# Optimization experiments

Measured on AMD Instinct MI355X. Metric: run time of the kernel, lower is better.

The kernel has to match this reference:

```python
import jax, jax.numpy as jnp
import numpy as np

B, S, D, K = 8, 2048, 1024, 204  # K = int(0.1 * seq_len)
LN_EPS = 1e-12


def setup_inputs() -> dict:
    key = jax.random.key(0)
    ks = jax.random.split(key, 8)
    scale = 0.02
    return {
        "input_tensor": jax.random.normal(ks[0], (B, S, D), jnp.float32),
        "attention_mask": jnp.zeros((B, 1, 1, S), jnp.float32),  # unused by module
        "Wq": jax.random.normal(ks[1], (D, K), jnp.float32) * scale,
        "bq": jnp.zeros((K,), jnp.float32),
        "Wk": jax.random.normal(ks[2], (D, K), jnp.float32) * scale,
        "bk": jnp.zeros((K,), jnp.float32),
        "Wv": jax.random.normal(ks[3], (D, D), jnp.float32) * scale,
        "bv": jnp.zeros((D,), jnp.float32),
        "Wd": jax.random.normal(ks[4], (D, D), jnp.float32) * scale,
        "bd": jnp.zeros((D,), jnp.float32),
        "gamma": jnp.ones((D,), jnp.float32),
        "beta": jnp.zeros((D,), jnp.float32),
    }


def reference(input_tensor, attention_mask, Wq, bq, Wk, bk, Wv, bv, Wd, bd, gamma, beta):
    # factorized synthesizer: low-rank (k=204) Q/K projections
    q = input_tensor @ Wq + bq          # [B,S,K]
    k = input_tensor @ Wk + bk          # [B,S,K]
    v = input_tensor @ Wv + bv          # [B,S,D]
    scores = jnp.einsum('bsk,btk->bst', q, k)          # [B,S,S]
    probs = jax.nn.softmax(scores, axis=-1)
    # per-head matmul with broadcast probs == direct matmul on merged heads
    ctx = jnp.einsum('bst,btd->bsd', probs, v)          # [B,S,D]
    h = ctx @ Wd + bd
    y = h + input_tensor                                 # residual
    mean = jnp.mean(y, axis=-1, keepdims=True)
    var = jnp.mean(jnp.square(y - mean), axis=-1, keepdims=True)
    return gamma * (y - mean) / jnp.sqrt(var + LN_EPS) + beta
```

## Files before the change

### kernel.cpp

```cpp
#include <hip/hip_runtime.h>
#include <stdint.h>

#define BB 8
#define SS 2048
#define DD 1024
#define KREAL 204

typedef __attribute__((ext_vector_type(8))) short short8;
typedef __attribute__((ext_vector_type(4))) float floatx4;
typedef uint16_t u16;
typedef uint32_t u32;

__device__ __forceinline__ float bf2f(u16 u) {
    union { float f; u32 i; } c; c.i = ((u32)u) << 16; return c.f;
}
__device__ __forceinline__ u16 f2bf(float f) {
    union { float f; u32 i; } c; c.f = f;
    u32 i = c.i;
    u32 r = (i + 0x7FFFu + ((i >> 16) & 1u)) >> 16;
    return (u16)r;
}

#if defined(__has_builtin)
#if __has_builtin(__builtin_amdgcn_global_load_lds)
#define HAVE_GLL 1
#endif
#endif

__device__ __forceinline__ void gload16(const u16* g, u16* l) {
#ifdef HAVE_GLL
    __builtin_amdgcn_global_load_lds(
        (const __attribute__((address_space(1))) void*)(uintptr_t)g,
        (__attribute__((address_space(3))) void*)(u32)(uintptr_t)(void*)l,
        16, 0, 0);
#else
    *(uint4*)l = *(const uint4*)g;
#endif
}

#define VM_WAIT(N) asm volatile("s_waitcnt vmcnt(" #N ")" ::: "memory")
#define S_BAR()    asm volatile("s_barrier" ::: "memory")

__device__ __forceinline__ void stage64(const u16* __restrict__ src, size_t ld,
                                        u16* lds, int tid) {
#pragma unroll
    for (int j = 0; j < 2; j++) {
        int flat = j * 256 + tid;
        int row = flat >> 3, slot = flat & 7;
        int kg = slot ^ (row & 7);
        gload16(src + (size_t)row * ld + kg * 8, lds + flat * 8);
    }
}
__device__ __forceinline__ short8 frag(const u16* lds, int row, int kslot) {
    return *(const short8*)&lds[(row << 6) + (((kslot ^ (row & 7)) & 7) << 3)];
}

__device__ __forceinline__ short8 frag32(const u16* plane, int row, int ks) {
    return *(const short8*)&plane[(row << 5) + (((ks ^ ((row >> 1) & 3)) & 3) << 3)];
}

__device__ __forceinline__ void stage_half(const u16* s0, const u16* s1,
                                           u16* dp, int tid) {
    gload16(s0, dp + tid * 8);
    gload16(s1, dp + 4096 + tid * 8);
}

template <int MT, bool LOADB>
__device__ __forceinline__ void phase16(const u16* Apl, const u16* Bpl,
                                        int arow, int brow, int ln, int quad,
                                        short8 (&bv)[4], floatx4 (&acc)[8][4]) {
    short8 af[4];
#pragma unroll
    for (int i = 0; i < 4; i++) af[i] = frag32(Apl, arow + (MT + i) * 16 + ln, quad);
    if (LOADB) {
#pragma unroll
        for (int nt = 0; nt < 4; nt++) bv[nt] = frag32(Bpl, brow + nt * 16 + ln, quad);
    }
    __builtin_amdgcn_s_setprio(1);
#pragma unroll
    for (int i = 0; i < 4; i++)
#pragma unroll
        for (int nt = 0; nt < 4; nt++)
            acc[MT + i][nt] = __builtin_amdgcn_mfma_f32_16x16x32_bf16(
                af[i], bv[nt], acc[MT + i][nt], 0, 0, 0);
    __builtin_amdgcn_s_setprio(0);
}

template <int NT>
__device__ __forceinline__ void gemm_core256(
    const u16* __restrict__ Ag, size_t lda,
    const u16* __restrict__ Bg, size_t ldb,
    u16* lds, int tid, floatx4 (&acc)[8][4]) {
    const int lane = tid & 63, w = tid >> 6;
    const int arow = (w >> 2) * 128, brow = (w & 3) * 64;
    const int ln = lane & 15, quad = lane >> 4;
    const int srow = tid >> 2;
    const int kgp = (tid & 3) ^ ((srow >> 1) & 3);
    const u16* A0 = Ag + (size_t)srow * lda + kgp * 8;
    const u16* A1 = Ag + (size_t)(srow + 128) * lda + kgp * 8;
    const u16* B0 = Bg + (size_t)srow * ldb + kgp * 8;
    const u16* B1 = Bg + (size_t)(srow + 128) * ldb + kgp * 8;
    u16* Al = lds;
    u16* Bl = lds + 32768;

    stage_half(A0,      A1,      Al,         tid);
    stage_half(B0,      B1,      Bl,         tid);
    stage_half(A0 + 32, A1 + 32, Al + 8192,  tid);
    stage_half(B0 + 32, B1 + 32, Bl + 8192,  tid);
    stage_half(A0 + 64, A1 + 64, Al + 16384, tid);
    stage_half(B0 + 64, B1 + 64, Bl + 16384, tid);

    short8 bv[4];
#pragma unroll 2
    for (int t = 0; t < NT - 1; ++t) {
        const int p  = (t & 1) * 2;
        const int pn = 2 - p;
        const u16* Ap0 = Al + p * 8192;
        const u16* Ap1 = Al + p * 8192 + 8192;
        const u16* Bp0 = Bl + p * 8192;
        const u16* Bp1 = Bl + p * 8192 + 8192;
        const size_t o1 = (size_t)(t + 1) * 64;
        const size_t o2 = (size_t)(t + 2) * 64;
        VM_WAIT(8); S_BAR();
        stage_half(A0 + o1 + 32, A1 + o1 + 32, Al + (pn + 1) * 8192, tid);
        phase16<0, true >(Ap0, Bp0, arow, brow, ln, quad, bv, acc);
        stage_half(B0 + o1 + 32, B1 + o1 + 32, Bl + (pn + 1) * 8192, tid);
        phase16<4, false>(Ap0, Bp0, arow, brow, ln, quad, bv, acc);
        VM_WAIT(8); S_BAR();
        if (t + 2 < NT) stage_half(A0 + o2, A1 + o2, Al + p * 8192, tid);
        phase16<0, true >(Ap1, Bp1, arow, brow, ln, quad, bv, acc);
        if (t + 2 < NT) stage_half(B0 + o2, B1 + o2, Bl + p * 8192, tid);
        phase16<4, false>(Ap1, Bp1, arow, brow, ln, quad, bv, acc);
    }
    {
        const int p = ((NT - 1) & 1) * 2;
        const u16* Ap0 = Al + p * 8192;
        const u16* Ap1 = Al + p * 8192 + 8192;
        const u16* Bp0 = Bl + p * 8192;
        const u16* Bp1 = Bl + p * 8192 + 8192;
        VM_WAIT(4); S_BAR();
        phase16<0, true >(Ap0, Bp0, arow, brow, ln, quad, bv, acc);
        phase16<4, false>(Ap0, Bp0, arow, brow, ln, quad, bv, acc);
        VM_WAIT(0); S_BAR();
        phase16<0, true >(Ap1, Bp1, arow, brow, ln, quad, bv, acc);
        phase16<4, false>(Ap1, Bp1, arow, brow, ln, quad, bv, acc);
    }
}

template <typename F>
__device__ __forceinline__ void store_rm256(u16* smem, u16* gbase, size_t ldc,
                                            int wm, int wn, int ln, int quad,
                                            int tid, F val) {
    for (int half = 0; half < 2; half++) {
        __syncthreads();
        if (wm == half) {
#pragma unroll
            for (int mt = 0; mt < 8; mt++)
#pragma unroll
                for (int nt = 0; nt < 4; nt++)
#pragma unroll
                    for (int r = 0; r < 4; r++)
                        smem[(mt * 16 + quad * 4 + r) * 264 + wn * 64 + nt * 16 + ln] =
                            val(mt, nt, r);
        }
        __syncthreads();
#pragma unroll
        for (int j = 0; j < 8; j++) {
            int flat = j * 512 + tid;
            int row = flat >> 5, c = flat & 31;
            *(uint4*)&gbase[(size_t)(half * 128 + row) * ldc + c * 8] =
                *(const uint4*)&smem[row * 264 + c * 8];
        }
    }
}

template <typename F4>
__device__ __forceinline__ void store_tr256(u16* smem, u16* gbase, size_t ldg,
                                            int wm, int wn, int ln, int quad,
                                            int tid, F4 val4) {
    for (int qr = 0; qr < 4; qr++) {
        __syncthreads();
        if (wn == qr) {
#pragma unroll
            for (int mt = 0; mt < 8; mt++)
#pragma unroll
                for (int nt = 0; nt < 4; nt++) {
                    ushort4 v = val4(mt, nt);
                    *(ushort4*)&smem[(nt * 16 + ln) * 264 + wm * 128 + mt * 16 + quad * 4] = v;
                }
        }
        __syncthreads();
#pragma unroll
        for (int j = 0; j < 4; j++) {
            int flat = j * 512 + tid;
            int c = flat >> 5, r8 = flat & 31;
            *(uint4*)&gbase[(size_t)(qr * 64 + c) * ldg + r8 * 8] =
                *(const uint4*)&smem[c * 264 + r8 * 8];
        }
    }
}

template <typename F>
__device__ __forceinline__ void store_rm256_f32(float* smem, float* gbase, size_t ldc,
                                                int wm, int wn, int ln, int quad,
                                                int tid, F val) {
    for (int c4 = 0; c4 < 4; c4++) {
        __syncthreads();
        if (wm == (c4 >> 1)) {
#pragma unroll
            for (int i = 0; i < 4; i++)
#pragma unroll
                for (int nt = 0; nt < 4; nt++)
#pragma unroll
                    for (int r = 0; r < 4; r++)
                        smem[(i * 16 + quad * 4 + r) * 260 + wn * 64 + nt * 16 + ln] =
                            val((c4 & 1) * 4 + i, nt, r);
        }
        __syncthreads();
#pragma unroll
        for (int j = 0; j < 8; j++) {
            int flat = j * 512 + tid;
            int row = flat >> 6, q = flat & 63;
            *(float4*)&gbase[(size_t)(c4 * 64 + row) * ldc + q * 4] =
                *(const float4*)&smem[row * 260 + q * 4];
        }
    }
}

__global__ __launch_bounds__(256) void k_cast_bf16(
    const float* __restrict__ x, u16* __restrict__ o) {
    size_t i = ((size_t)blockIdx.x * 256 + threadIdx.x) * 4;
    float4 v = *(const float4*)&x[i];
    ushort4 p;
    p.x = f2bf(v.x); p.y = f2bf(v.y); p.z = f2bf(v.z); p.w = f2bf(v.w);
    *(ushort4*)&o[i] = p;
}

__global__ __launch_bounds__(256) void k_prep(
    const float* __restrict__ Wq, const float* __restrict__ Wk,
    const float* __restrict__ Wv, const float* __restrict__ Wd,
    const float* __restrict__ bv, const float* __restrict__ bd,
    const float* __restrict__ bq, const float* __restrict__ bk,
    u16* __restrict__ Wqkt, u16* __restrict__ Wv16, u16* __restrict__ Wdt,
    float* __restrict__ bc, float* __restrict__ bqk) {
    const int z = blockIdx.z;
    const int t = threadIdx.x;
    if (z == 4) {
        int id = blockIdx.y * 32 + blockIdx.x;
        if (id < 16) {
            __shared__ float red[4][64];
            int n = id * 64 + (t & 63);
            int dc = t >> 6;
            float s = 0.f;
            for (int d = dc * 256; d < dc * 256 + 256; d++)
                s += bv[d] * Wd[(size_t)d * 1024 + n];
            red[dc][t & 63] = s;
            __syncthreads();
            if (dc == 0) bc[n] = bd[n] + red[0][t & 63] + red[1][t & 63] + red[2][t & 63] + red[3][t & 63];
        } else if (id == 16) {
            for (int i = t; i < 512; i += 256) {
                float v = 0.f;
                if (i < KREAL) v = bq[i];
                else if (i >= 256 && i < 256 + KREAL) v = bk[i - 256];
                bqk[i] = v;
            }
        }
        return;
    }
    __shared__ u16 tile[32][33];
    int k0 = blockIdx.x * 32, n0 = blockIdx.y * 32;
    int tx = t & 31, ty = t >> 5;
    if (z == 2) {
        for (int i = ty; i < 32; i += 8) {
            size_t idx = (size_t)(k0 + i) * 1024 + n0 + tx;
            Wv16[idx] = f2bf(Wv[idx]);
        }
        return;
    }
    const float* W; u16* out; int N, Npad, rowoff;
    if (z == 0)      { W = Wq; out = Wqkt; N = KREAL; Npad = 256;  rowoff = 0;   }
    else if (z == 1) { W = Wk; out = Wqkt; N = KREAL; Npad = 256;  rowoff = 256; }
    else             { W = Wd; out = Wdt;  N = 1024;  Npad = 1024; rowoff = 0;   }
    if (n0 >= Npad) return;
    for (int i = ty; i < 32; i += 8) {
        int n = n0 + tx;
        tile[i][tx] = (n < N) ? f2bf(W[(size_t)(k0 + i) * N + n]) : (u16)0;
    }
    __syncthreads();
    for (int i = ty; i < 32; i += 8) {
        int n = n0 + i;
        if (n < Npad) out[(size_t)(rowoff + n) * 1024 + k0 + tx] = tile[tx][i];
    }
}

__global__ __launch_bounds__(256) void k_gemm64(
    const u16* __restrict__ A, const u16* __restrict__ Bt,
    u16* __restrict__ C, int ldc) {
    __shared__ u16 As[64 * 64];
    __shared__ u16 Bs[64 * 64];
    const int tid = threadIdx.x;
    const int m0 = blockIdx.x * 64, n0 = blockIdx.y * 64;
    const int lane = tid & 63, w = tid >> 6;
    const int ln = lane & 15, quad = lane >> 4;

    floatx4 acc[4];
    floatx4 zero = {0.f, 0.f, 0.f, 0.f};
#pragma unroll
    for (int nt = 0; nt < 4; nt++) acc[nt] = zero;

    for (int kt = 0; kt < 16; kt++) {
        __syncthreads();
        stage64(A + (size_t)m0 * 1024 + kt * 64, 1024, As, tid);
        stage64(Bt + (size_t)n0 * 1024 + kt * 64, 1024, Bs, tid);
        __syncthreads();
#pragma unroll
        for (int kk = 0; kk < 2; kk++) {
            short8 av = frag(As, w * 16 + ln, kk * 4 + quad);
#pragma unroll
            for (int nt = 0; nt < 4; nt++) {
                short8 bvf = frag(Bs, nt * 16 + ln, kk * 4 + quad);
                acc[nt] = __builtin_amdgcn_mfma_f32_16x16x32_bf16(av, bvf, acc[nt], 0, 0, 0);
            }
        }
    }
    const int row0 = m0 + w * 16 + quad * 4;
#pragma unroll
    for (int nt = 0; nt < 4; nt++) {
        const int col = n0 + nt * 16 + ln;
        ushort4 pk;
        pk.x = f2bf(acc[nt][0]); pk.y = f2bf(acc[nt][1]);
        pk.z = f2bf(acc[nt][2]); pk.w = f2bf(acc[nt][3]);
        *reinterpret_cast<ushort4*>(&C[(size_t)col * ldc + row0]) = pk;
    }
}

__global__ __launch_bounds__(512, 2) void k_proj2(
    const u16* __restrict__ A, const u16* __restrict__ Wqkt,
    const u16* __restrict__ Wvdt, const float* __restrict__ bqk,
    u16* __restrict__ qkp, u16* __restrict__ ut) {
    __shared__ __align__(16) u16 lds[65536];
    const int tid = threadIdx.x;
    const int m0 = blockIdx.x * 256;
    const int by = blockIdx.y;
    const int lane = tid & 63, w = tid >> 6;
    const int wm = w >> 2, wn = w & 3;
    const int ln = lane & 15, quad = lane >> 4;

    floatx4 acc[8][4];
    floatx4 zero = {0.f, 0.f, 0.f, 0.f};
#pragma unroll
    for (int mt = 0; mt < 8; mt++)
#pragma unroll
        for (int nt = 0; nt < 4; nt++) acc[mt][nt] = zero;

    const u16* Ag = A + (size_t)m0 * 1024;
    const int n0 = (by < 2) ? by * 256 : (by - 2) * 256;
    const u16* Bg = (by < 2) ? (Wqkt + (size_t)n0 * 1024) : (Wvdt + (size_t)n0 * 1024);
    gemm_core256<16>(Ag, 1024, Bg, 1024, lds, tid, acc);

    if (by < 2) {
        float b4[4];
#pragma unroll
        for (int nt = 0; nt < 4; nt++) b4[nt] = bqk[n0 + wn * 64 + nt * 16 + ln];
        store_rm256(lds, qkp + (size_t)m0 * 512 + n0, 512, wm, wn, ln, quad, tid,
            [&](int mt, int nt, int r) -> u16 {
                return f2bf(acc[mt][nt][r] + b4[nt]);
            });
    } else {
        int b = m0 >> 11, s0loc = m0 & 2047;
        store_tr256(lds, ut + ((size_t)b * DD + n0) * SS + s0loc, SS, wm, wn, ln, quad, tid,
            [&](int mt, int nt) -> ushort4 {
                ushort4 pk;
                pk.x = f2bf(acc[mt][nt][0]); pk.y = f2bf(acc[mt][nt][1]);
                pk.z = f2bf(acc[mt][nt][2]); pk.w = f2bf(acc[mt][nt][3]);
                return pk;
            });
    }
}

__global__ __launch_bounds__(512, 2) void k_qk2(
    const u16* __restrict__ qkp, u16* __restrict__ P, float* __restrict__ lg) {
    __shared__ __align__(16) u16 lds[65536];
    const int tid = threadIdx.x;
    const int s0 = blockIdx.x * 256, t0 = blockIdx.y * 256, bb = blockIdx.z;
    const int lane = tid & 63, w = tid >> 6;
    const int wm = w >> 2, wn = w & 3;
    const int ln = lane & 15, quad = lane >> 4;

    floatx4 acc[8][4];
    floatx4 zero = {0.f, 0.f, 0.f, 0.f};
#pragma unroll
    for (int mt = 0; mt < 8; mt++)
#pragma unroll
        for (int nt = 0; nt < 4; nt++) acc[mt][nt] = zero;

    gemm_core256<4>(qkp + ((size_t)bb * SS + s0) * 512, 512,
                    qkp + ((size_t)bb * SS + t0) * 512 + 256, 512, lds, tid, acc);

#pragma unroll
    for (int mt = 0; mt < 8; mt++)
#pragma unroll
        for (int nt = 0; nt < 4; nt++)
#pragma unroll
            for (int r = 0; r < 4; r++)
                acc[mt][nt][r] = __expf(acc[mt][nt][r] - 30.f);

#pragma unroll
    for (int mt = 0; mt < 8; mt++) {
#pragma unroll
        for (int r = 0; r < 4; r++) {
            float rs = acc[mt][0][r] + acc[mt][1][r] + acc[mt][2][r] + acc[mt][3][r];
            rs += __shfl_xor(rs, 1);
            rs += __shfl_xor(rs, 2);
            rs += __shfl_xor(rs, 4);
            rs += __shfl_xor(rs, 8);
            if (ln == 0)
                atomicAdd(&lg[(size_t)bb * SS + s0 + wm * 128 + mt * 16 + quad * 4 + r], rs);
        }
    }

    store_rm256(lds, P + (size_t)bb * SS * SS + (size_t)s0 * SS + t0, SS,
                wm, wn, ln, quad, tid,
        [&](int mt, int nt, int r) -> u16 { return f2bf(acc[mt][nt][r]); });
}

__global__ __launch_bounds__(512, 2) void k_h2(
    const u16* __restrict__ P, const u16* __restrict__ ut,
    const float* __restrict__ lg, const float* __restrict__ bc,
    const float* __restrict__ xres, float* __restrict__ out) {
    __shared__ __align__(16) u16 lds[65536];
    const int tid = threadIdx.x;
    const int s0 = blockIdx.x * 256, d0 = blockIdx.y * 256, bb = blockIdx.z;
    const int lane = tid & 63, w = tid >> 6;
    const int wm = w >> 2, wn = w & 3;
    const int ln = lane & 15, quad = lane >> 4;

    floatx4 acc[8][4];
    floatx4 zero = {0.f, 0.f, 0.f, 0.f};
#pragma unroll
    for (int mt = 0; mt < 8; mt++)
#pragma unroll
        for (int nt = 0; nt < 4; nt++) acc[mt][nt] = zero;

    gemm_core256<32>(P + ((size_t)bb * SS + s0) * SS, SS,
                     ut + ((size_t)bb * DD + d0) * SS, SS, lds, tid, acc);

    float b4[4];
#pragma unroll
    for (int nt = 0; nt < 4; nt++) b4[nt] = bc[d0 + wn * 64 + nt * 16 + ln];
    float inv[8][4];
#pragma unroll
    for (int mt = 0; mt < 8; mt++)
#pragma unroll
        for (int r = 0; r < 4; r++)
            inv[mt][r] = 1.f / lg[(size_t)bb * SS + s0 + wm * 128 + mt * 16 + quad * 4 + r];

    store_rm256_f32((float*)lds, out + ((size_t)bb * SS + s0) * DD + d0, DD,
                    wm, wn, ln, quad, tid,
        [&](int mt, int nt, int r) -> float {
            size_t grow = (size_t)bb * SS + s0 + wm * 128 + mt * 16 + quad * 4 + r;
            int col = d0 + wn * 64 + nt * 16 + ln;
            return acc[mt][nt][r] * inv[mt][r] + b4[nt] + xres[grow * DD + col];
        });
}

__global__ __launch_bounds__(256) void k_ln_f32(
    float* __restrict__ io, const float* __restrict__ gamma,
    const float* __restrict__ beta) {
    const int tid = threadIdx.x;
    const int lane = tid & 63, w = tid >> 6;
    const size_t row = (size_t)blockIdx.x * 4 + w;
    float* rp = io + row * DD;

    float v[16];
#pragma unroll
    for (int j = 0; j < 4; j++) {
        float4 t = *(const float4*)&rp[j * 256 + lane * 4];
        v[j * 4 + 0] = t.x; v[j * 4 + 1] = t.y; v[j * 4 + 2] = t.z; v[j * 4 + 3] = t.w;
    }
    float s = 0.f, sq = 0.f;
#pragma unroll
    for (int i = 0; i < 16; i++) { s += v[i]; sq += v[i] * v[i]; }
#pragma unroll
    for (int msk = 1; msk < 64; msk <<= 1) {
        s  += __shfl_xor(s,  msk, 64);
        sq += __shfl_xor(sq, msk, 64);
    }
    float mean = s * (1.f / 1024.f);
    float var  = sq * (1.f / 1024.f) - mean * mean;
    float rstd = rsqrtf(fmaxf(var, 0.f) + 1e-12f);
#pragma unroll
    for (int j = 0; j < 4; j++) {
        float4 g  = *(const float4*)&gamma[j * 256 + lane * 4];
        float4 bt = *(const float4*)&beta [j * 256 + lane * 4];
        float4 o;
        o.x = g.x * (v[j * 4 + 0] - mean) * rstd + bt.x;
        o.y = g.y * (v[j * 4 + 1] - mean) * rstd + bt.y;
        o.z = g.z * (v[j * 4 + 2] - mean) * rstd + bt.z;
        o.w = g.w * (v[j * 4 + 3] - mean) * rstd + bt.w;
        *(float4*)&rp[j * 256 + lane * 4] = o;
    }
}

extern "C" void kernel_launch(void* const* d_in, const int* in_sizes, int n_in,
                              void* d_out, int out_size, void* d_ws, size_t ws_size,
                              hipStream_t stream) {
    const float* x     = (const float*)d_in[0];
    const float* Wq    = (const float*)d_in[2];
    const float* bq    = (const float*)d_in[3];
    const float* Wk    = (const float*)d_in[4];
    const float* bk    = (const float*)d_in[5];
    const float* Wv    = (const float*)d_in[6];
    const float* bv    = (const float*)d_in[7];
    const float* Wd    = (const float*)d_in[8];
    const float* bd    = (const float*)d_in[9];
    const float* gamma = (const float*)d_in[10];
    const float* beta  = (const float*)d_in[11];
    float* out = (float*)d_out;

    char* ws = (char*)d_ws;
    u16*   qkp  = (u16*)(ws + 0);
    u16*   ut   = (u16*)(ws + 16777216);
    u16*   P    = (u16*)(ws + 50331648);
    u16*   x16  = (u16*)(ws + 50331648);
    u16*   Wv16 = (u16*)(ws + 83886080);
    u16*   Wvdt = (u16*)(ws + 85983232);
    u16*   Wdt  = (u16*)(ws + 88080384);
    u16*   Wqkt = (u16*)(ws + 90177536);
    float* lg   = (float*)(ws + 117440512);
    float* bc   = (float*)(ws + 117506048);
    float* bqk  = (float*)(ws + 117510144);

    k_cast_bf16<<<dim3(16384), dim3(256), 0, stream>>>(x, x16);
    k_prep<<<dim3(32, 32, 5), dim3(256), 0, stream>>>(Wq, Wk, Wv, Wd, bv, bd, bq, bk,
                                                      Wqkt, Wv16, Wdt, bc, bqk);
    k_gemm64<<<dim3(16, 16), dim3(256), 0, stream>>>(Wv16, Wdt, Wvdt, 1024);

    k_proj2<<<dim3(64, 6), dim3(512), 0, stream>>>(x16, Wqkt, Wvdt, bqk, qkp, ut);

    hipMemsetAsync(lg, 0, (size_t)BB * SS * sizeof(float), stream);

    k_qk2<<<dim3(8, 8, 8), dim3(512), 0, stream>>>(qkp, P, lg);
    k_h2 <<<dim3(8, 4, 8), dim3(512), 0, stream>>>(P, ut, lg, bc, x, out);

    k_ln_f32<<<dim3(4096), dim3(256), 0, stream>>>(out, gamma, beta);
}
```

Baseline: 361.7 us.

## Swizzle block order for L2 locality and coalesce residual epilogue reads

Remaps the linear block index in the projection, QK and PV GEMM kernels so that consecutively launched blocks share the same A or B operand tiles, aiming for better L2/MALL reuse (likely across XCDs on MI355X). The k_h2 epilogue is also reworked: the fp32 accumulator is staged through LDS first, and the bias, residual and 1/rowsum scaling are then applied in the coalesced float4 store phase. Previously the residual was read with scattered per-element loads inside the accumulator loop. The remapping depends on fixed grid dimensions.

```diff
diff --git a/kernel.cpp b/kernel.cpp
--- a/kernel.cpp
+++ b/kernel.cpp
@@ -196,33 +196,6 @@
             int c = flat >> 5, r8 = flat & 31;
             *(uint4*)&gbase[(size_t)(qr * 64 + c) * ldg + r8 * 8] =
                 *(const uint4*)&smem[c * 264 + r8 * 8];
-        }
-    }
-}
-
-template <typename F>
-__device__ __forceinline__ void store_rm256_f32(float* smem, float* gbase, size_t ldc,
-                                                int wm, int wn, int ln, int quad,
-                                                int tid, F val) {
-    for (int c4 = 0; c4 < 4; c4++) {
-        __syncthreads();
-        if (wm == (c4 >> 1)) {
-#pragma unroll
-            for (int i = 0; i < 4; i++)
-#pragma unroll
-                for (int nt = 0; nt < 4; nt++)
-#pragma unroll
-                    for (int r = 0; r < 4; r++)
-                        smem[(i * 16 + quad * 4 + r) * 260 + wn * 64 + nt * 16 + ln] =
-                            val((c4 & 1) * 4 + i, nt, r);
-        }
-        __syncthreads();
-#pragma unroll
-        for (int j = 0; j < 8; j++) {
-            int flat = j * 512 + tid;
-            int row = flat >> 6, q = flat & 63;
-            *(float4*)&gbase[(size_t)(c4 * 64 + row) * ldc + q * 4] =
-                *(const float4*)&smem[row * 260 + q * 4];
         }
     }
 }
@@ -340,8 +313,10 @@
     u16* __restrict__ qkp, u16* __restrict__ ut) {
     __shared__ __align__(16) u16 lds[65536];
     const int tid = threadIdx.x;
-    const int m0 = blockIdx.x * 256;
-    const int by = blockIdx.y;
+    int lin = blockIdx.x + (blockIdx.y << 6);
+    int l = (lin & 7) * 48 + (lin >> 3);
+    const int by = l % 6;
+    const int m0 = (l / 6) * 256;
     const int lane = tid & 63, w = tid >> 6;
     const int wm = w >> 2, wn = w & 3;
     const int ln = lane & 15, quad = lane >> 4;
@@ -382,7 +357,10 @@
     const u16* __restrict__ qkp, u16* __restrict__ P, float* __restrict__ lg) {
     __shared__ __align__(16) u16 lds[65536];
     const int tid = threadIdx.x;
-    const int s0 = blockIdx.x * 256, t0 = blockIdx.y * 256, bb = blockIdx.z;
+    int lin = blockIdx.x + (blockIdx.y << 3) + (blockIdx.z << 6);
+    int l = ((lin & 7) << 6) + (lin >> 3);
+    const int bb = l >> 6, rem = l & 63;
+    const int s0 = (rem & 7) * 256, t0 = (rem >> 3) * 256;
     const int lane = tid & 63, w = tid >> 6;
     const int wm = w >> 2, wn = w & 3;
     const int ln = lane & 15, quad = lane >> 4;
@@ -430,7 +408,10 @@
     const float* __restrict__ xres, float* __restrict__ out) {
     __shared__ __align__(16) u16 lds[65536];
     const int tid = threadIdx.x;
-    const int s0 = blockIdx.x * 256, d0 = blockIdx.y * 256, bb = blockIdx.z;
+    int lin = blockIdx.x + (blockIdx.y << 3) + (blockIdx.z << 5);
+    int l = ((lin & 7) << 5) + (lin >> 3);
+    const int bb = l >> 5, rem = l & 31;
+    const int s0 = (rem & 7) * 256, d0 = (rem >> 3) * 256;
     const int lane = tid & 63, w = tid >> 6;
     const int wm = w >> 2, wn = w & 3;
     const int ln = lane & 15, quad = lane >> 4;
@@ -445,23 +426,39 @@
     gemm_core256<32>(P + ((size_t)bb * SS + s0) * SS, SS,
                      ut + ((size_t)bb * DD + d0) * SS, SS, lds, tid, acc);
 
-    float b4[4];
-#pragma unroll
-    for (int nt = 0; nt < 4; nt++) b4[nt] = bc[d0 + wn * 64 + nt * 16 + ln];
-    float inv[8][4];
-#pragma unroll
-    for (int mt = 0; mt < 8; mt++)
-#pragma unroll
-        for (int r = 0; r < 4; r++)
-            inv[mt][r] = 1.f / lg[(size_t)bb * SS + s0 + wm * 128 + mt * 16 + quad * 4 + r];
-
-    store_rm256_f32((float*)lds, out + ((size_t)bb * SS + s0) * DD + d0, DD,
-                    wm, wn, ln, quad, tid,
-        [&](int mt, int nt, int r) -> float {
-            size_t grow = (size_t)bb * SS + s0 + wm * 128 + mt * 16 + quad * 4 + r;
-            int col = d0 + wn * 64 + nt * 16 + ln;
-            return acc[mt][nt][r] * inv[mt][r] + b4[nt] + xres[grow * DD + col];
-        });
+    float* smem = (float*)lds;
+    float* outb = out + ((size_t)bb * SS + s0) * DD + d0;
+    const float* xb = xres + ((size_t)bb * SS + s0) * DD + d0;
+    for (int c4 = 0; c4 < 4; c4++) {
+        __syncthreads();
+        if (wm == (c4 >> 1)) {
+#pragma unroll
+            for (int i = 0; i < 4; i++)
+#pragma unroll
+                for (int nt = 0; nt < 4; nt++)
+#pragma unroll
+                    for (int r = 0; r < 4; r++)
+                        smem[(i * 16 + quad * 4 + r) * 260 + wn * 64 + nt * 16 + ln] =
+                            acc[(c4 & 1) * 4 + i][nt][r];
+        }
+        __syncthreads();
+#pragma unroll
+        for (int j = 0; j < 8; j++) {
+            int flat = j * 512 + tid;
+            int row = flat >> 6, q = flat & 63;
+            size_t grow = (size_t)bb * SS + s0 + c4 * 64 + row;
+            float iv = 1.f / lg[grow];
+            float4 a  = *(const float4*)&smem[row * 260 + q * 4];
+            float4 b4 = *(const float4*)&bc[d0 + q * 4];
+            float4 xr = *(const float4*)&xb[(size_t)(c4 * 64 + row) * DD + q * 4];
+            float4 o;
+            o.x = a.x * iv + b4.x + xr.x;
+            o.y = a.y * iv + b4.y + xr.y;
+            o.z = a.z * iv + b4.z + xr.z;
+            o.w = a.w * iv + b4.w + xr.w;
+            *(float4*)&outb[(size_t)(c4 * 64 + row) * DD + q * 4] = o;
+        }
+    }
 }
 
 __global__ __launch_bounds__(256) void k_ln_f32(
```

Measured after the change: 428.5 us. +18.5%, slower.
